# Performance work log

Measured on AMD Instinct MI355X. Metric: run time of the kernel, lower is better.

## Reference

```python
import jax, jax.numpy as jnp
import numpy as np
import math

IN_DIM = 512
LR_MUL = 1.0
SCALE = (1.0 / math.sqrt(IN_DIM)) * LR_MUL  # EqualLinear runtime weight scale


def setup_inputs() -> dict:
    key = jax.random.key(0)
    k1, k2 = jax.random.split(key)
    x = jax.random.normal(k1, (256, 18, 18, 512), dtype=jnp.float32)  # [B, n_out, n_layers, in_dim]
    W = jax.random.normal(k2, (18, 512, 512), dtype=jnp.float32)      # [n_out, out_dim, in_dim]
    b = jnp.zeros((18, 512), dtype=jnp.float32)                        # [n_out, out_dim], bias_init=0
    idx = jnp.arange(18, dtype=jnp.int32)                              # n_indx
    return {"x": x, "W": W, "b": b, "idx": idx}


def reference(x, W, b, idx):
    # Fused equivalent of the nested loops: for each direction i, apply
    # EqualLinear_i to slices x[:, i, j, :] for j in idx, writing results back.
    x_sel = x[:, :, idx, :]                                    # [B, O, J, D_in]
    y = jnp.einsum('koji,odi->kojd', x_sel, W) * SCALE         # [B, O, J, D_out]
    y = y + (b * LR_MUL)[None, :, None, :]
    return x.at[:, :, idx, :].set(y)
```

## Files before the change

### kernel.cpp

```cpp
#include <hip/hip_runtime.h>
#include <hip/hip_bf16.h>


typedef __bf16  bf16x8  __attribute__((ext_vector_type(8)));
typedef float   floatx4 __attribute__((ext_vector_type(4)));

#define O_DIM 18
#define J_DIM 18
#define KB    256
#define C_DIM 512
#define BM    128
#define BN    128
#define BK    32
#define NK    (C_DIM / BK)
#define LDSS  40

__device__ __forceinline__ __bf16 f2bf(float f) { return (__bf16)f; }

__global__ __launch_bounds__(256, 3)
void dirnet_gemm(const float* __restrict__ x, const float* __restrict__ W,
                 const float* __restrict__ bias, const int* __restrict__ idx,
                 float* __restrict__ out)
{
    const int id   = blockIdx.x;
    const int xcd  = id & 7;
    const int slot = id >> 3;
    const int nt   = slot & 3;
    const int g    = (slot >> 2) * 8 + xcd;
    const int mt   = g & 1;
    const int jo   = g >> 1;
    const int j    = jo % J_DIM;
    const int o    = jo / J_DIM;
    const int jj   = idx[j];

    __shared__ __bf16 As[2][BM * LDSS];
    __shared__ __bf16 Bs[2][BM * LDSS];

    const int tid  = threadIdx.x;
    const int srow = tid >> 2;
    const int scol = (tid & 3) << 3;

    const size_t xRow0      = ((size_t)((mt * BM + srow) * O_DIM + o) * J_DIM + jj) * C_DIM;
    const size_t xRowStride = (size_t)64 * O_DIM * J_DIM * C_DIM;
    const size_t wRow0      = ((size_t)(o * C_DIM + nt * BN + srow)) * C_DIM;
    const size_t wRowStride = (size_t)64 * C_DIM;

    const int lane = tid & 63;
    const int wv   = tid >> 6;
    const int mOff = (wv & 1) * 64;
    const int nOff = (wv >> 1) * 64;
    const int lrow = lane & 15;
    const int lk   = (lane >> 4) << 3;

    floatx4 acc[4][4] = {};
    float4 pa[2][2], pb[2][2];

    #pragma unroll
    for (int p = 0; p < 2; ++p) {
        const float* ap = x + xRow0 + (size_t)p * xRowStride + scol;
        pa[p][0] = *(const float4*)ap;
        pa[p][1] = *(const float4*)(ap + 4);
        const float* bp = W + wRow0 + (size_t)p * wRowStride + scol;
        pb[p][0] = *(const float4*)bp;
        pb[p][1] = *(const float4*)(bp + 4);
    }

    for (int t = 0; t < NK; ++t) {
        const int cur = t & 1;

        #pragma unroll
        for (int p = 0; p < 2; ++p) {
            bf16x8 sa;
            sa[0]=f2bf(pa[p][0].x); sa[1]=f2bf(pa[p][0].y);
            sa[2]=f2bf(pa[p][0].z); sa[3]=f2bf(pa[p][0].w);
            sa[4]=f2bf(pa[p][1].x); sa[5]=f2bf(pa[p][1].y);
            sa[6]=f2bf(pa[p][1].z); sa[7]=f2bf(pa[p][1].w);
            *(bf16x8*)&As[cur][(p * 64 + srow) * LDSS + scol] = sa;

            bf16x8 sb;
            sb[0]=f2bf(pb[p][0].x); sb[1]=f2bf(pb[p][0].y);
            sb[2]=f2bf(pb[p][0].z); sb[3]=f2bf(pb[p][0].w);
            sb[4]=f2bf(pb[p][1].x); sb[5]=f2bf(pb[p][1].y);
            sb[6]=f2bf(pb[p][1].z); sb[7]=f2bf(pb[p][1].w);
            *(bf16x8*)&Bs[cur][(p * 64 + srow) * LDSS + scol] = sb;
        }

        __syncthreads();

        if (t + 1 < NK) {
            const int k0 = (t + 1) * BK;
            #pragma unroll
            for (int p = 0; p < 2; ++p) {
                const float* ap = x + xRow0 + (size_t)p * xRowStride + k0 + scol;
                pa[p][0] = *(const float4*)ap;
                pa[p][1] = *(const float4*)(ap + 4);
                const float* bp = W + wRow0 + (size_t)p * wRowStride + k0 + scol;
                pb[p][0] = *(const float4*)bp;
                pb[p][1] = *(const float4*)(bp + 4);
            }
        }

        bf16x8 af[4], bfr[4];
        #pragma unroll
        for (int mi = 0; mi < 4; ++mi)
            af[mi] = *(const bf16x8*)&As[cur][(mOff + mi * 16 + lrow) * LDSS + lk];
        #pragma unroll
        for (int ni = 0; ni < 4; ++ni)
            bfr[ni] = *(const bf16x8*)&Bs[cur][(nOff + ni * 16 + lrow) * LDSS + lk];

        #pragma unroll
        for (int mi = 0; mi < 4; ++mi)
            #pragma unroll
            for (int ni = 0; ni < 4; ++ni)
                acc[mi][ni] = __builtin_amdgcn_mfma_f32_16x16x32_bf16(
                    af[mi], bfr[ni], acc[mi][ni], 0, 0, 0);
    }

    const float scale = 0.04419417382415922f;
    const int rbase = (lane >> 4) << 2;
    #pragma unroll
    for (int ni = 0; ni < 4; ++ni) {
        const int d  = nt * BN + nOff + ni * 16 + lrow;
        const float bv = bias[o * C_DIM + d];
        #pragma unroll
        for (int mi = 0; mi < 4; ++mi) {
            #pragma unroll
            for (int r = 0; r < 4; ++r) {
                const int kr = mt * BM + mOff + mi * 16 + rbase + r;
                __builtin_nontemporal_store(
                    acc[mi][ni][r] * scale + bv,
                    &out[((size_t)(kr * O_DIM + o) * J_DIM + jj) * C_DIM + d]);
            }
        }
    }
}

__global__ void copy_nonsel(const float* __restrict__ x, const int* __restrict__ idx,
                            float* __restrict__ out)
{
    const int jj = blockIdx.x;
    const int o  = blockIdx.y;
    bool member = false;
    for (int t = 0; t < J_DIM; ++t) member = member || (idx[t] == jj);
    if (member) return;
    const int tid = threadIdx.x;
    for (int k = 0; k < KB; ++k) {
        const size_t base = ((size_t)(k * O_DIM + o) * J_DIM + jj) * C_DIM;
        for (int c = tid * 4; c < C_DIM; c += 256 * 4) {
            *(float4*)&out[base + c] = *(const float4*)&x[base + c];
        }
    }
}

extern "C" void kernel_launch(void* const* d_in, const int* in_sizes, int n_in,
                              void* d_out, int out_size, void* d_ws, size_t ws_size,
                              hipStream_t stream) {
    const float* x   = (const float*)d_in[0];
    const float* W   = (const float*)d_in[1];
    const float* b   = (const float*)d_in[2];
    const int*   idx = (const int*)d_in[3];
    float* out = (float*)d_out;

    dirnet_gemm<<<dim3(8 * J_DIM * O_DIM), 256, 0, stream>>>(x, W, b, idx, out);
    copy_nonsel<<<dim3(J_DIM, O_DIM), 256, 0, stream>>>(x, idx, out);
}
```

Measured before the change: 423.2 us.

## Prefetch x two K-steps ahead, single-buffer LDS with split barriers

Register prefetching of the x tile now runs two K iterations ahead while W stays one ahead. The LDS double buffer is replaced by a single buffer guarded by two explicit waitcnt+barrier pairs per step. The loop is fully unrolled, occupancy hint drops from 3 to 2 waves per SIMD, and the epilogue uses plain stores instead of nontemporal ones. The aim is to hide more global-load latency on the memory-bound x stream, at the cost of more registers, lower occupancy and an extra barrier per iteration.

```diff
diff --git a/kernel.cpp b/kernel.cpp
--- a/kernel.cpp
+++ b/kernel.cpp
@@ -17,7 +17,12 @@
 
 __device__ __forceinline__ __bf16 f2bf(float f) { return (__bf16)f; }
 
-__global__ __launch_bounds__(256, 3)
+__device__ __forceinline__ void barrier_lds() {
+    __builtin_amdgcn_s_waitcnt(0xc07f);
+    __builtin_amdgcn_s_barrier();
+}
+
+__global__ __launch_bounds__(256, 2)
 void dirnet_gemm(const float* __restrict__ x, const float* __restrict__ W,
                  const float* __restrict__ bias, const int* __restrict__ idx,
                  float* __restrict__ out)
@@ -33,17 +38,17 @@
     const int o    = jo / J_DIM;
     const int jj   = idx[j];
 
-    __shared__ __bf16 As[2][BM * LDSS];
-    __shared__ __bf16 Bs[2][BM * LDSS];
+    __shared__ __bf16 As[BM * LDSS];
+    __shared__ __bf16 Bs[BN * LDSS];
 
     const int tid  = threadIdx.x;
     const int srow = tid >> 2;
     const int scol = (tid & 3) << 3;
 
-    const size_t xRow0      = ((size_t)((mt * BM + srow) * O_DIM + o) * J_DIM + jj) * C_DIM;
-    const size_t xRowStride = (size_t)64 * O_DIM * J_DIM * C_DIM;
-    const size_t wRow0      = ((size_t)(o * C_DIM + nt * BN + srow)) * C_DIM;
-    const size_t wRowStride = (size_t)64 * C_DIM;
+    const float* xp = x + ((size_t)((mt * BM + srow) * O_DIM + o) * J_DIM + jj) * C_DIM + scol;
+    const size_t xRS = (size_t)64 * O_DIM * J_DIM * C_DIM;
+    const float* wp = W + ((size_t)(o * C_DIM + nt * BN + srow)) * C_DIM + scol;
+    const size_t wRS = (size_t)64 * C_DIM;
 
     const int lane = tid & 63;
     const int wv   = tid >> 6;
@@ -53,60 +58,77 @@
     const int lk   = (lane >> 4) << 3;
 
     floatx4 acc[4][4] = {};
-    float4 pa[2][2], pb[2][2];
+    float4 pa[2][2][2];
+    float4 pb[2][2];
 
     #pragma unroll
     for (int p = 0; p < 2; ++p) {
-        const float* ap = x + xRow0 + (size_t)p * xRowStride + scol;
-        pa[p][0] = *(const float4*)ap;
-        pa[p][1] = *(const float4*)(ap + 4);
-        const float* bp = W + wRow0 + (size_t)p * wRowStride + scol;
-        pb[p][0] = *(const float4*)bp;
-        pb[p][1] = *(const float4*)(bp + 4);
+        pb[p][0] = *(const float4*)(wp + p * wRS);
+        pb[p][1] = *(const float4*)(wp + p * wRS + 4);
+    }
+    #pragma unroll
+    for (int p = 0; p < 2; ++p) {
+        pa[0][p][0] = *(const float4*)(xp + p * xRS);
+        pa[0][p][1] = *(const float4*)(xp + p * xRS + 4);
+    }
+    #pragma unroll
+    for (int p = 0; p < 2; ++p) {
+        pa[1][p][0] = *(const float4*)(xp + p * xRS + BK);
+        pa[1][p][1] = *(const float4*)(xp + p * xRS + BK + 4);
     }
 
+    #pragma unroll
     for (int t = 0; t < NK; ++t) {
-        const int cur = t & 1;
+        const int s = t & 1;
 
+        bf16x8 sa[2], sb[2];
         #pragma unroll
         for (int p = 0; p < 2; ++p) {
-            bf16x8 sa;
-            sa[0]=f2bf(pa[p][0].x); sa[1]=f2bf(pa[p][0].y);
-            sa[2]=f2bf(pa[p][0].z); sa[3]=f2bf(pa[p][0].w);
-            sa[4]=f2bf(pa[p][1].x); sa[5]=f2bf(pa[p][1].y);
-            sa[6]=f2bf(pa[p][1].z); sa[7]=f2bf(pa[p][1].w);
-            *(bf16x8*)&As[cur][(p * 64 + srow) * LDSS + scol] = sa;
-
-            bf16x8 sb;
-            sb[0]=f2bf(pb[p][0].x); sb[1]=f2bf(pb[p][0].y);
-            sb[2]=f2bf(pb[p][0].z); sb[3]=f2bf(pb[p][0].w);
-            sb[4]=f2bf(pb[p][1].x); sb[5]=f2bf(pb[p][1].y);
-            sb[6]=f2bf(pb[p][1].z); sb[7]=f2bf(pb[p][1].w);
-            *(bf16x8*)&Bs[cur][(p * 64 + srow) * LDSS + scol] = sb;
+            sa[p][0]=f2bf(pa[s][p][0].x); sa[p][1]=f2bf(pa[s][p][0].y);
+            sa[p][2]=f2bf(pa[s][p][0].z); sa[p][3]=f2bf(pa[s][p][0].w);
+            sa[p][4]=f2bf(pa[s][p][1].x); sa[p][5]=f2bf(pa[s][p][1].y);
+            sa[p][6]=f2bf(pa[s][p][1].z); sa[p][7]=f2bf(pa[s][p][1].w);
+        }
+        #pragma unroll
+        for (int p = 0; p < 2; ++p) {
+            sb[p][0]=f2bf(pb[p][0].x); sb[p][1]=f2bf(pb[p][0].y);
+            sb[p][2]=f2bf(pb[p][0].z); sb[p][3]=f2bf(pb[p][0].w);
+            sb[p][4]=f2bf(pb[p][1].x); sb[p][5]=f2bf(pb[p][1].y);
+            sb[p][6]=f2bf(pb[p][1].z); sb[p][7]=f2bf(pb[p][1].w);
         }
 
-        __syncthreads();
+        barrier_lds();
+        #pragma unroll
+        for (int p = 0; p < 2; ++p) {
+            *(bf16x8*)&As[(p * 64 + srow) * LDSS + scol] = sa[p];
+            *(bf16x8*)&Bs[(p * 64 + srow) * LDSS + scol] = sb[p];
+        }
+        barrier_lds();
 
         if (t + 1 < NK) {
-            const int k0 = (t + 1) * BK;
+            const int k1 = (t + 1) * BK;
             #pragma unroll
             for (int p = 0; p < 2; ++p) {
-                const float* ap = x + xRow0 + (size_t)p * xRowStride + k0 + scol;
-                pa[p][0] = *(const float4*)ap;
-                pa[p][1] = *(const float4*)(ap + 4);
-                const float* bp = W + wRow0 + (size_t)p * wRowStride + k0 + scol;
-                pb[p][0] = *(const float4*)bp;
-                pb[p][1] = *(const float4*)(bp + 4);
+                pb[p][0] = *(const float4*)(wp + p * wRS + k1);
+                pb[p][1] = *(const float4*)(wp + p * wRS + k1 + 4);
+            }
+        }
+        if (t + 2 < NK) {
+            const int k2 = (t + 2) * BK;
+            #pragma unroll
+            for (int p = 0; p < 2; ++p) {
+                pa[s][p][0] = *(const float4*)(xp + p * xRS + k2);
+                pa[s][p][1] = *(const float4*)(xp + p * xRS + k2 + 4);
             }
         }
 
         bf16x8 af[4], bfr[4];
         #pragma unroll
         for (int mi = 0; mi < 4; ++mi)
-            af[mi] = *(const bf16x8*)&As[cur][(mOff + mi * 16 + lrow) * LDSS + lk];
+            af[mi] = *(const bf16x8*)&As[(mOff + mi * 16 + lrow) * LDSS + lk];
         #pragma unroll
         for (int ni = 0; ni < 4; ++ni)
-            bfr[ni] = *(const bf16x8*)&Bs[cur][(nOff + ni * 16 + lrow) * LDSS + lk];
+            bfr[ni] = *(const bf16x8*)&Bs[(nOff + ni * 16 + lrow) * LDSS + lk];
 
         #pragma unroll
         for (int mi = 0; mi < 4; ++mi)
@@ -127,9 +149,8 @@
             #pragma unroll
             for (int r = 0; r < 4; ++r) {
                 const int kr = mt * BM + mOff + mi * 16 + rbase + r;
-                __builtin_nontemporal_store(
-                    acc[mi][ni][r] * scale + bv,
-                    &out[((size_t)(kr * O_DIM + o) * J_DIM + jj) * C_DIM + d]);
+                out[((size_t)(kr * O_DIM + o) * J_DIM + jj) * C_DIM + d] =
+                    acc[mi][ni][r] * scale + bv;
             }
         }
     }
@@ -161,6 +182,6 @@
     const int*   idx = (const int*)d_in[3];
     float* out = (float*)d_out;
 
-    dirnet_gemm<<<dim3(8 * J_DIM * O_DIM), 256, 0, stream>>>(x, W, b, idx, out);
+    dirnet_gemm<<<dim3(2 * 4 * J_DIM * O_DIM), 256, 0, stream>>>(x, W, b, idx, out);
     copy_nonsel<<<dim3(J_DIM, O_DIM), 256, 0, stream>>>(x, idx, out);
 }
```

Measured after the change: 367.6 us. 1.15x faster.
